# Kernel tuning notes

Hardware: AMD Instinct MI355X
Metric: run time of the kernel (lower is better)

The kernel has to match this reference:

```python
import jax, jax.numpy as jnp
import numpy as np

B, N, D = 16, 1024, 768
H = 12
HD = D // H           # 64
NUM_BUCKETS = 49      # iRPE 'product' buckets, shared across heads
SCALE = HD ** -0.5


def setup_inputs() -> dict:
    key = jax.random.key(0)
    k1, k2, k3, k4, k5, k6 = jax.random.split(key, 6)
    x = jax.random.normal(k1, (B, N, D), dtype=jnp.float32)
    qkv_w = jax.random.normal(k2, (3 * D, D), dtype=jnp.float32) * 0.02
    rpe_table = jax.random.normal(k3, (NUM_BUCKETS, HD), dtype=jnp.float32) * 0.02
    rp_bucket = jax.random.randint(k4, (N, N), 0, NUM_BUCKETS, dtype=jnp.int32)
    proj_w = jax.random.normal(k5, (D, D), dtype=jnp.float32) * 0.02
    proj_b = jax.random.normal(k6, (D,), dtype=jnp.float32) * 0.02
    return {"x": x, "qkv_w": qkv_w, "rpe_table": rpe_table,
            "rp_bucket": rp_bucket, "proj_w": proj_w, "proj_b": proj_b}


def reference(x, qkv_w, rpe_table, rp_bucket, proj_w, proj_b):
    b, n, d = x.shape
    # qkv projection (no bias), split into q,k,v of shape [B,H,N,HD]
    qkv = (x @ qkv_w.T).reshape(b, n, 3, H, HD)
    qkv = jnp.transpose(qkv, (2, 0, 3, 1, 4))
    q, k, v = qkv[0], qkv[1], qkv[2]
    q = q * SCALE
    # full attention scores [B,H,N,N]
    attn = jnp.einsum('bhid,bhjd->bhij', q, k)
    # iRPE contextual bias on keys: project q onto the bucket table, then
    # gather per relative-position bucket: bias[b,h,i,j] = (q @ W^T)[b,h,i,rp_bucket[i,j]]
    bias_all = jnp.einsum('bhid,cd->bhic', q, rpe_table)   # [B,H,N,num_buckets]
    bias = bias_all[:, :, jnp.arange(n)[:, None], rp_bucket]  # [B,H,N,N]
    attn = jax.nn.softmax(attn + bias, axis=-1)
    out = jnp.einsum('bhij,bhjd->bhid', attn, v)            # [B,H,N,HD]
    out = jnp.transpose(out, (0, 2, 1, 3)).reshape(b, n, d)
    return out @ proj_w.T + proj_b
```

## Files before the change

kernel.cpp:

```cpp
#include <hip/hip_runtime.h>

typedef short bf16x8 __attribute__((ext_vector_type(8)));
typedef float f32x4 __attribute__((ext_vector_type(4)));

#define QSCALE 0.1803368801111204f

__device__ __forceinline__ unsigned short f2bf(float f){
  unsigned u = __float_as_uint(f);
  u = (u + 0x7fffu + ((u >> 16) & 1u)) >> 16;
  return (unsigned short)u;
}
__device__ __forceinline__ f32x4 mfma16(bf16x8 a, bf16x8 b, f32x4 c){
  return __builtin_amdgcn_mfma_f32_16x16x32_bf16(a, b, c, 0, 0, 0);
}
__device__ __forceinline__ void gload_lds16(const void* g, void* l){
  __builtin_amdgcn_global_load_lds((__attribute__((address_space(1))) void*)(g),
                                   (__attribute__((address_space(3))) void*)(l), 16, 0, 0);
}
__device__ __forceinline__ unsigned cvt_pk_bf16(float lo, float hi){
  unsigned r;
  asm("v_cvt_pk_bf16_f32 %0, %1, %2" : "=v"(r) : "v"(lo), "v"(hi));
  return r;
}
__device__ __forceinline__ float exp2_fast(float x){
  float r;
  asm("v_exp_f32 %0, %1" : "=v"(r) : "v"(x));
  return r;
}

__global__ __launch_bounds__(256) void prep_kernel(
    const float* __restrict__ x, const float* __restrict__ qw,
    const float* __restrict__ pw, const int* __restrict__ rp,
    unsigned short* __restrict__ xb, unsigned short* __restrict__ wb,
    unsigned short* __restrict__ pwb, unsigned char* __restrict__ rp8){
  const int T1 = 3145728;
  const int T2 = T1 + 442368;
  const int T3 = T2 + 147456;
  const int T4 = T3 + 262144;
  for (int t = blockIdx.x * 256 + threadIdx.x; t < T4; t += gridDim.x * 256){
    if (t < T3){
      const float4* src; ushort4* dst; int off;
      if (t < T1){ src = (const float4*)x;  dst = (ushort4*)xb;  off = t; }
      else if (t < T2){ src = (const float4*)qw; dst = (ushort4*)wb;  off = t - T1; }
      else { src = (const float4*)pw; dst = (ushort4*)pwb; off = t - T2; }
      float4 v = src[off];
      ushort4 u;
      u.x = f2bf(v.x); u.y = f2bf(v.y); u.z = f2bf(v.z); u.w = f2bf(v.w);
      dst[off] = u;
    } else {
      int off = t - T3;
      int4 v = ((const int4*)rp)[off];
      int row = (off * 4) >> 10;
      int sw = (row & 7) << 4;
      uchar4 u;
      u.x = (unsigned char)((v.x << 2) ^ sw);
      u.y = (unsigned char)((v.y << 2) ^ sw);
      u.z = (unsigned char)((v.z << 2) ^ sw);
      u.w = (unsigned char)((v.w << 2) ^ sw);
      ((uchar4*)rp8)[off] = u;
    }
  }
}

__device__ __forceinline__ void gemm_core(
    const unsigned short* __restrict__ A, const unsigned short* __restrict__ Bm,
    int m0, int n0, int K, unsigned short* As, unsigned short* Bs,
    f32x4 (&acc)[4][4]){
  const int tid = threadIdx.x, lane = tid & 63, wave = tid >> 6;
  const int g = lane >> 4, r16 = lane & 15;
  const int wr = wave >> 1, wc = wave & 1;
  for (int k0 = 0; k0 < K; k0 += 32){
    __syncthreads();
    #pragma unroll
    for (int j = 0; j < 2; j++){
      int ci = j * 256 + tid;
      int row = ci >> 2, c = ci & 3;
      gload_lds16(A  + (size_t)(m0 + row) * K + k0 + c * 8,
                  (char*)As + (j * 256 + wave * 64) * 16);
      gload_lds16(Bm + (size_t)(n0 + row) * K + k0 + c * 8,
                  (char*)Bs + (j * 256 + wave * 64) * 16);
    }
    __syncthreads();
    bf16x8 a[4], b[4];
    #pragma unroll
    for (int mi = 0; mi < 4; mi++)
      a[mi] = *(const bf16x8*)((const char*)As + (wr * 64 + mi * 16 + r16) * 64 + g * 16);
    #pragma unroll
    for (int ni = 0; ni < 4; ni++)
      b[ni] = *(const bf16x8*)((const char*)Bs + (wc * 64 + ni * 16 + r16) * 64 + g * 16);
    #pragma unroll
    for (int mi = 0; mi < 4; mi++)
      #pragma unroll
      for (int ni = 0; ni < 4; ni++)
        acc[mi][ni] = mfma16(a[mi], b[ni], acc[mi][ni]);
  }
}

__global__ __launch_bounds__(256) void qkv_gemm(
    const unsigned short* __restrict__ xb, const unsigned short* __restrict__ wb,
    unsigned short* __restrict__ q_s, unsigned short* __restrict__ k_s,
    unsigned short* __restrict__ v_t){
  __shared__ __align__(16) unsigned short As[128 * 32];
  __shared__ __align__(16) unsigned short Bs[128 * 32];
  f32x4 acc[4][4];
  #pragma unroll
  for (int i = 0; i < 4; i++)
    #pragma unroll
    for (int j = 0; j < 4; j++){
      acc[i][j][0] = 0.f; acc[i][j][1] = 0.f; acc[i][j][2] = 0.f; acc[i][j][3] = 0.f;
    }
  const int m0 = blockIdx.y * 128, n0 = blockIdx.x * 128;
  gemm_core(xb, wb, m0, n0, 768, As, Bs, acc);

  const int lane = threadIdx.x & 63, wave = threadIdx.x >> 6;
  const int g = lane >> 4, r16 = lane & 15;
  const int wr = wave >> 1, wc = wave & 1;
  #pragma unroll
  for (int mi = 0; mi < 4; mi++){
    #pragma unroll
    for (int ni = 0; ni < 4; ni++){
      int gcol = n0 + wc * 64 + ni * 16 + r16;
      int sel = gcol / 768;
      int rem = gcol - sel * 768;
      int h = rem >> 6, hd = rem & 63;
      #pragma unroll
      for (int r = 0; r < 4; r++){
        int grow = m0 + wr * 64 + mi * 16 + 4 * g + r;
        int bb = grow >> 10, ii = grow & 1023;
        size_t base = ((size_t)(bb * 12 + h)) << 16;
        float v = acc[mi][ni][r];
        if (sel == 0)      q_s[base + ((size_t)ii << 6) + hd] = f2bf(v * QSCALE);
        else if (sel == 1) k_s[base + ((size_t)ii << 6) + hd] = f2bf(v);
        else               v_t[base + ((size_t)hd << 10) + ii] = f2bf(v);
      }
    }
  }
}

__global__ __launch_bounds__(256) void attn_kernel(
    const unsigned short* __restrict__ q_s, const unsigned short* __restrict__ k_s,
    const unsigned short* __restrict__ v_t, const unsigned char* __restrict__ rp8,
    const float* __restrict__ rpe, unsigned short* __restrict__ ao){
  __shared__ __align__(16) char smem[40960];
  const int tid = threadIdx.x, lane = tid & 63, w = tid >> 6;
  const int g = lane >> 4, r16 = lane & 15;
  const int qb = blockIdx.x, bh = blockIdx.y;
  const size_t bh_base = (size_t)bh << 16;

  const int i_loc = w * 16 + r16;
  const size_t qoff = bh_base + ((size_t)(qb * 64 + i_loc) << 6);
  bf16x8 qf0 = *(const bf16x8*)(q_s + qoff + g * 8);
  bf16x8 qf1 = *(const bf16x8*)(q_s + qoff + 32 + g * 8);

  float* bias_lds = (float*)(smem + 24576);
  const int s4 = (i_loc & 7) << 2;
  #pragma unroll
  for (int jt = 0; jt < 4; jt++){
    int row = jt * 16 + r16;
    bf16x8 a0, a1;
    #pragma unroll
    for (int e = 0; e < 8; e++){ a0[e] = 0; a1[e] = 0; }
    if (row < 49){
      const float* rr = rpe + row * 64 + g * 8;
      float4 x0 = *(const float4*)(rr);
      float4 x1 = *(const float4*)(rr + 4);
      float4 y0 = *(const float4*)(rr + 32);
      float4 y1 = *(const float4*)(rr + 36);
      a0[0]=f2bf(x0.x); a0[1]=f2bf(x0.y); a0[2]=f2bf(x0.z); a0[3]=f2bf(x0.w);
      a0[4]=f2bf(x1.x); a0[5]=f2bf(x1.y); a0[6]=f2bf(x1.z); a0[7]=f2bf(x1.w);
      a1[0]=f2bf(y0.x); a1[1]=f2bf(y0.y); a1[2]=f2bf(y0.z); a1[3]=f2bf(y0.w);
      a1[4]=f2bf(y1.x); a1[5]=f2bf(y1.y); a1[6]=f2bf(y1.z); a1[7]=f2bf(y1.w);
    }
    f32x4 z = {0.f, 0.f, 0.f, 0.f};
    z = mfma16(a0, qf0, z);
    z = mfma16(a1, qf1, z);
    *(f32x4*)(bias_lds + i_loc * 64 + ((jt * 16 + 4 * g) ^ s4)) = z;
  }

  unsigned short* ks = (unsigned short*)smem;
  unsigned short* vs = (unsigned short*)(smem + 8192);
  char* pbuf = smem + 16384 + w * 2048;
  const char* browb = (const char*)bias_lds + i_loc * 256;

  const int ci0 = tid, ci1 = 256 + tid;
  const int row0 = ci0 >> 3, sc0 = (ci0 & 7) ^ (row0 & 7);
  const int row1 = ci1 >> 3, sc1 = (ci1 & 7) ^ (row1 & 7);
  const char* kp0 = (const char*)(k_s + bh_base) + row0 * 128 + sc0 * 16;
  const char* kp1 = (const char*)(k_s + bh_base) + row1 * 128 + sc1 * 16;
  const char* vp0 = (const char*)(v_t + bh_base) + row0 * 2048 + sc0 * 16;
  const char* vp1 = (const char*)(v_t + bh_base) + row1 * 2048 + sc1 * 16;
  char* kl0 = (char*)smem + w * 1024;
  char* kl1 = (char*)smem + 4096 + w * 1024;
  char* vl0 = (char*)smem + 8192 + w * 1024;
  char* vl1 = (char*)smem + 12288 + w * 1024;
  const unsigned char* rprow = rp8 + ((size_t)(qb * 64 + i_loc) << 10);

  f32x4 o[4];
  #pragma unroll
  for (int dt = 0; dt < 4; dt++){ o[dt][0]=0.f; o[dt][1]=0.f; o[dt][2]=0.f; o[dt][3]=0.f; }
  float m_i = -INFINITY, l_i = 0.f;

  for (int kb = 0; kb < 16; kb++){
    __syncthreads();
    gload_lds16(kp0, kl0);
    gload_lds16(kp1, kl1);
    gload_lds16(vp0, vl0);
    gload_lds16(vp1, vl1);
    kp0 += 8192; kp1 += 8192; vp0 += 128; vp1 += 128;
    __syncthreads();

    f32x4 st[4];
    #pragma unroll
    for (int jt = 0; jt < 4; jt++){
      int krow = jt * 16 + r16;
      int sw = (krow & 7) << 4;
      bf16x8 ka0 = *(const bf16x8*)((char*)ks + krow * 128 + ((g * 16) ^ sw));
      bf16x8 ka1 = *(const bf16x8*)((char*)ks + krow * 128 + ((64 + g * 16) ^ sw));
      f32x4 z = {0.f, 0.f, 0.f, 0.f};
      z = mfma16(ka0, qf0, z);
      z = mfma16(ka1, qf1, z);
      st[jt] = z;
    }
    #pragma unroll
    for (int jt = 0; jt < 4; jt++){
      unsigned bu = *(const unsigned*)(rprow + kb * 64 + jt * 16 + g * 4);
      st[jt][0] += *(const float*)(browb + (bu & 0xff));
      st[jt][1] += *(const float*)(browb + ((bu >> 8) & 0xff));
      st[jt][2] += *(const float*)(browb + ((bu >> 16) & 0xff));
      st[jt][3] += *(const float*)(browb + (bu >> 24));
    }
    float tmax = -INFINITY;
    #pragma unroll
    for (int jt = 0; jt < 4; jt++)
      tmax = fmaxf(tmax, fmaxf(fmaxf(st[jt][0], st[jt][1]), fmaxf(st[jt][2], st[jt][3])));
    tmax = fmaxf(tmax, __shfl_xor(tmax, 16));
    tmax = fmaxf(tmax, __shfl_xor(tmax, 32));
    const bool skip = __all(tmax <= m_i + 8.f);
    float mnew = m_i, alpha;
    if (!skip){
      mnew = fmaxf(m_i, tmax);
      alpha = exp2_fast(m_i - mnew);
    }
    float psum = 0.f;
    #pragma unroll
    for (int jt = 0; jt < 4; jt++){
      float p0 = exp2_fast(st[jt][0] - mnew);
      float p1 = exp2_fast(st[jt][1] - mnew);
      float p2 = exp2_fast(st[jt][2] - mnew);
      float p3 = exp2_fast(st[jt][3] - mnew);
      psum += (p0 + p1) + (p2 + p3);
      uint2 u; u.x = cvt_pk_bf16(p0, p1); u.y = cvt_pk_bf16(p2, p3);
      *(uint2*)(pbuf + r16 * 128 + ((jt * 32 + g * 8) ^ ((r16 & 7) << 4))) = u;
    }
    psum += __shfl_xor(psum, 16);
    psum += __shfl_xor(psum, 32);
    if (!skip){
      l_i = l_i * alpha + psum;
      float af[4];
      #pragma unroll
      for (int r = 0; r < 4; r++) af[r] = __shfl(alpha, 4 * g + r);
      #pragma unroll
      for (int dt = 0; dt < 4; dt++){
        o[dt][0] *= af[0]; o[dt][1] *= af[1]; o[dt][2] *= af[2]; o[dt][3] *= af[3];
      }
    } else {
      l_i += psum;
    }
    m_i = mnew;
    #pragma unroll
    for (int kt = 0; kt < 2; kt++){
      bf16x8 pa = *(const bf16x8*)(pbuf + r16 * 128 + ((kt * 64 + g * 16) ^ ((r16 & 7) << 4)));
      #pragma unroll
      for (int dt = 0; dt < 4; dt++){
        int vrow = dt * 16 + r16;
        bf16x8 vb = *(const bf16x8*)((char*)vs + vrow * 128 + ((kt * 64 + g * 16) ^ ((vrow & 7) << 4)));
        o[dt] = mfma16(pa, vb, o[dt]);
      }
    }
  }

  float lf[4];
  #pragma unroll
  for (int r = 0; r < 4; r++) lf[r] = 1.f / __shfl(l_i, 4 * g + r);
  const int bidx = bh / 12, h = bh - bidx * 12;
  #pragma unroll
  for (int dt = 0; dt < 4; dt++){
    int d = dt * 16 + r16;
    #pragma unroll
    for (int r = 0; r < 4; r++){
      int i = qb * 64 + w * 16 + 4 * g + r;
      ao[(size_t)(bidx * 1024 + i) * 768 + h * 64 + d] = f2bf(o[dt][r] * lf[r]);
    }
  }
}

__global__ __launch_bounds__(256) void proj_gemm(
    const unsigned short* __restrict__ aob, const unsigned short* __restrict__ pwb,
    const float* __restrict__ pb, float* __restrict__ out){
  __shared__ __align__(16) unsigned short As[128 * 32];
  __shared__ __align__(16) unsigned short Bs[128 * 32];
  f32x4 acc[4][4];
  #pragma unroll
  for (int i = 0; i < 4; i++)
    #pragma unroll
    for (int j = 0; j < 4; j++){
      acc[i][j][0] = 0.f; acc[i][j][1] = 0.f; acc[i][j][2] = 0.f; acc[i][j][3] = 0.f;
    }
  const int m0 = blockIdx.y * 128, n0 = blockIdx.x * 128;
  gemm_core(aob, pwb, m0, n0, 768, As, Bs, acc);

  const int lane = threadIdx.x & 63, wave = threadIdx.x >> 6;
  const int g = lane >> 4, r16 = lane & 15;
  const int wr = wave >> 1, wc = wave & 1;
  #pragma unroll
  for (int mi = 0; mi < 4; mi++){
    #pragma unroll
    for (int ni = 0; ni < 4; ni++){
      int gcol = n0 + wc * 64 + ni * 16 + r16;
      float bias = pb[gcol];
      #pragma unroll
      for (int r = 0; r < 4; r++){
        int grow = m0 + wr * 64 + mi * 16 + 4 * g + r;
        out[(size_t)grow * 768 + gcol] = acc[mi][ni][r] + bias;
      }
    }
  }
}

extern "C" void kernel_launch(void* const* d_in, const int* in_sizes, int n_in,
                              void* d_out, int out_size, void* d_ws, size_t ws_size,
                              hipStream_t stream){
  const float* x      = (const float*)d_in[0];
  const float* qkv_w  = (const float*)d_in[1];
  const float* rpe    = (const float*)d_in[2];
  const int*   rp     = (const int*)d_in[3];
  const float* proj_w = (const float*)d_in[4];
  const float* proj_b = (const float*)d_in[5];
  float* out = (float*)d_out;
  char* ws = (char*)d_ws;

  unsigned short* xb  = (unsigned short*)(ws);
  unsigned short* wb  = (unsigned short*)(ws + 25165824);
  unsigned short* pwb = (unsigned short*)(ws + 28704768);
  unsigned char*  rp8 = (unsigned char*) (ws + 29884416);
  unsigned short* q_s = (unsigned short*)(ws + 30932992);
  unsigned short* k_s = (unsigned short*)(ws + 56098816);
  unsigned short* v_t = (unsigned short*)(ws + 81264640);
  unsigned short* aob = (unsigned short*)(ws + 106430464);

  prep_kernel<<<2048, 256, 0, stream>>>(x, qkv_w, proj_w, rp, xb, wb, pwb, rp8);
  qkv_gemm<<<dim3(18, 128), 256, 0, stream>>>(xb, wb, q_s, k_s, v_t);
  attn_kernel<<<dim3(16, 192), 256, 0, stream>>>(q_s, k_s, v_t, rp8, rpe, aob);
  proj_gemm<<<dim3(6, 128), 256, 0, stream>>>(aob, pwb, proj_b, out);
}
```

Baseline: 309.3 us.

## Process 32 query rows per wave in attention and store bias table as bf16

Each attention wave now handles two 16-row query tiles (128 queries per block, half as many blocks), so every K/V tile loaded into LDS is reused across twice as many queries, halving K/V global traffic and sync overhead per query. The per-row bucket bias table is stored in LDS as bf16 instead of fp32 (bucket indices pre-shifted by 1 instead of 2) so the larger query tile fits in LDS. The row-sum reduction is deferred to the end of the loop. Costs are more registers (8 accumulators, 4 Q fragments), larger LDS per block, fewer blocks for occupancy, and slightly lower bias precision.

New measurement: 307.1 us. About the same (-0.7%).

```diff
diff --git a/kernel.cpp b/kernel.cpp
--- a/kernel.cpp
+++ b/kernel.cpp
@@ -53,10 +53,10 @@
       int row = (off * 4) >> 10;
       int sw = (row & 7) << 4;
       uchar4 u;
-      u.x = (unsigned char)((v.x << 2) ^ sw);
-      u.y = (unsigned char)((v.y << 2) ^ sw);
-      u.z = (unsigned char)((v.z << 2) ^ sw);
-      u.w = (unsigned char)((v.w << 2) ^ sw);
+      u.x = (unsigned char)((v.x << 1) ^ sw);
+      u.y = (unsigned char)((v.y << 1) ^ sw);
+      u.z = (unsigned char)((v.z << 1) ^ sw);
+      u.w = (unsigned char)((v.w << 1) ^ sw);
       ((uchar4*)rp8)[off] = u;
     }
   }
@@ -141,27 +141,29 @@
     const unsigned short* __restrict__ q_s, const unsigned short* __restrict__ k_s,
     const unsigned short* __restrict__ v_t, const unsigned char* __restrict__ rp8,
     const float* __restrict__ rpe, unsigned short* __restrict__ ao){
-  __shared__ __align__(16) char smem[40960];
+  __shared__ __align__(16) char smem[49152];
   const int tid = threadIdx.x, lane = tid & 63, w = tid >> 6;
   const int g = lane >> 4, r16 = lane & 15;
   const int qb = blockIdx.x, bh = blockIdx.y;
   const size_t bh_base = (size_t)bh << 16;
-
-  const int i_loc = w * 16 + r16;
-  const size_t qoff = bh_base + ((size_t)(qb * 64 + i_loc) << 6);
-  bf16x8 qf0 = *(const bf16x8*)(q_s + qoff + g * 8);
-  bf16x8 qf1 = *(const bf16x8*)(q_s + qoff + 32 + g * 8);
-
-  float* bias_lds = (float*)(smem + 24576);
-  const int s4 = (i_loc & 7) << 2;
+  const int iw = w * 32;
+
+  const size_t q0 = bh_base + ((size_t)(qb * 128 + iw + r16) << 6);
+  bf16x8 qf[4];
+  qf[0] = *(const bf16x8*)(q_s + q0 + g * 8);
+  qf[1] = *(const bf16x8*)(q_s + q0 + 32 + g * 8);
+  qf[2] = *(const bf16x8*)(q_s + q0 + 1024 + g * 8);
+  qf[3] = *(const bf16x8*)(q_s + q0 + 1024 + 32 + g * 8);
+
+  char* bias_lds = smem + 32768;
   #pragma unroll
   for (int jt = 0; jt < 4; jt++){
-    int row = jt * 16 + r16;
+    int crow = jt * 16 + r16;
     bf16x8 a0, a1;
     #pragma unroll
     for (int e = 0; e < 8; e++){ a0[e] = 0; a1[e] = 0; }
-    if (row < 49){
-      const float* rr = rpe + row * 64 + g * 8;
+    if (crow < 49){
+      const float* rr = rpe + crow * 64 + g * 8;
       float4 x0 = *(const float4*)(rr);
       float4 x1 = *(const float4*)(rr + 4);
       float4 y0 = *(const float4*)(rr + 32);
@@ -171,16 +173,22 @@
       a1[0]=f2bf(y0.x); a1[1]=f2bf(y0.y); a1[2]=f2bf(y0.z); a1[3]=f2bf(y0.w);
       a1[4]=f2bf(y1.x); a1[5]=f2bf(y1.y); a1[6]=f2bf(y1.z); a1[7]=f2bf(y1.w);
     }
-    f32x4 z = {0.f, 0.f, 0.f, 0.f};
-    z = mfma16(a0, qf0, z);
-    z = mfma16(a1, qf1, z);
-    *(f32x4*)(bias_lds + i_loc * 64 + ((jt * 16 + 4 * g) ^ s4)) = z;
-  }
+    #pragma unroll
+    for (int h = 0; h < 2; h++){
+      f32x4 z = {0.f, 0.f, 0.f, 0.f};
+      z = mfma16(a0, qf[2 * h], z);
+      z = mfma16(a1, qf[2 * h + 1], z);
+      int irow = iw + h * 16 + r16;
+      uint2 u; u.x = cvt_pk_bf16(z[0], z[1]); u.y = cvt_pk_bf16(z[2], z[3]);
+      *(uint2*)(bias_lds + irow * 128 + ((jt * 32 + 8 * g) ^ ((r16 & 7) << 4))) = u;
+    }
+  }
+  const char* brow0 = bias_lds + (iw + r16) * 128;
+  const char* brow1 = brow0 + 16 * 128;
 
   unsigned short* ks = (unsigned short*)smem;
   unsigned short* vs = (unsigned short*)(smem + 8192);
-  char* pbuf = smem + 16384 + w * 2048;
-  const char* browb = (const char*)bias_lds + i_loc * 256;
+  char* pbuf = smem + 16384 + w * 4096;
 
   const int ci0 = tid, ci1 = 256 + tid;
   const int row0 = ci0 >> 3, sc0 = (ci0 & 7) ^ (row0 & 7);
@@ -193,12 +201,13 @@
   char* kl1 = (char*)smem + 4096 + w * 1024;
   char* vl0 = (char*)smem + 8192 + w * 1024;
   char* vl1 = (char*)smem + 12288 + w * 1024;
-  const unsigned char* rprow = rp8 + ((size_t)(qb * 64 + i_loc) << 10);
-
-  f32x4 o[4];
-  #pragma unroll
-  for (int dt = 0; dt < 4; dt++){ o[dt][0]=0.f; o[dt][1]=0.f; o[dt][2]=0.f; o[dt][3]=0.f; }
-  float m_i = -INFINITY, l_i = 0.f;
+  const unsigned char* rprow0 = rp8 + ((size_t)(qb * 128 + iw + r16) << 10);
+  const unsigned char* rprow1 = rprow0 + (16 << 10);
+
+  f32x4 o[8];
+  #pragma unroll
+  for (int t = 0; t < 8; t++){ o[t][0]=0.f; o[t][1]=0.f; o[t][2]=0.f; o[t][3]=0.f; }
+  float m0 = -INFINITY, m1 = -INFINITY, l0 = 0.f, l1 = 0.f;
 
   for (int kb = 0; kb < 16; kb++){
     __syncthreads();
@@ -209,87 +218,109 @@
     kp0 += 8192; kp1 += 8192; vp0 += 128; vp1 += 128;
     __syncthreads();
 
-    f32x4 st[4];
+    f32x4 st0[4], st1[4];
     #pragma unroll
     for (int jt = 0; jt < 4; jt++){
       int krow = jt * 16 + r16;
       int sw = (krow & 7) << 4;
       bf16x8 ka0 = *(const bf16x8*)((char*)ks + krow * 128 + ((g * 16) ^ sw));
       bf16x8 ka1 = *(const bf16x8*)((char*)ks + krow * 128 + ((64 + g * 16) ^ sw));
-      f32x4 z = {0.f, 0.f, 0.f, 0.f};
-      z = mfma16(ka0, qf0, z);
-      z = mfma16(ka1, qf1, z);
-      st[jt] = z;
+      f32x4 z0 = {0.f, 0.f, 0.f, 0.f};
+      z0 = mfma16(ka0, qf[0], z0);
+      z0 = mfma16(ka1, qf[1], z0);
+      st0[jt] = z0;
+      f32x4 z1 = {0.f, 0.f, 0.f, 0.f};
+      z1 = mfma16(ka0, qf[2], z1);
+      z1 = mfma16(ka1, qf[3], z1);
+      st1[jt] = z1;
     }
     #pragma unroll
     for (int jt = 0; jt < 4; jt++){
-      unsigned bu = *(const unsigned*)(rprow + kb * 64 + jt * 16 + g * 4);
-      st[jt][0] += *(const float*)(browb + (bu & 0xff));
-      st[jt][1] += *(const float*)(browb + ((bu >> 8) & 0xff));
-      st[jt][2] += *(const float*)(browb + ((bu >> 16) & 0xff));
-      st[jt][3] += *(const float*)(browb + (bu >> 24));
-    }
-    float tmax = -INFINITY;
-    #pragma unroll
-    for (int jt = 0; jt < 4; jt++)
-      tmax = fmaxf(tmax, fmaxf(fmaxf(st[jt][0], st[jt][1]), fmaxf(st[jt][2], st[jt][3])));
-    tmax = fmaxf(tmax, __shfl_xor(tmax, 16));
-    tmax = fmaxf(tmax, __shfl_xor(tmax, 32));
-    const bool skip = __all(tmax <= m_i + 8.f);
-    float mnew = m_i, alpha;
+      unsigned bu0 = *(const unsigned*)(rprow0 + kb * 64 + jt * 16 + g * 4);
+      unsigned bu1 = *(const unsigned*)(rprow1 + kb * 64 + jt * 16 + g * 4);
+      st0[jt][0] += __uint_as_float((unsigned)*(const unsigned short*)(brow0 + (bu0 & 0xff)) << 16);
+      st0[jt][1] += __uint_as_float((unsigned)*(const unsigned short*)(brow0 + ((bu0 >> 8) & 0xff)) << 16);
+      st0[jt][2] += __uint_as_float((unsigned)*(const unsigned short*)(brow0 + ((bu0 >> 16) & 0xff)) << 16);
+      st0[jt][3] += __uint_as_float((unsigned)*(const unsigned short*)(brow0 + (bu0 >> 24)) << 16);
+      st1[jt][0] += __uint_as_float((unsigned)*(const unsigned short*)(brow1 + (bu1 & 0xff)) << 16);
+      st1[jt][1] += __uint_as_float((unsigned)*(const unsigned short*)(brow1 + ((bu1 >> 8) & 0xff)) << 16);
+      st1[jt][2] += __uint_as_float((unsigned)*(const unsigned short*)(brow1 + ((bu1 >> 16) & 0xff)) << 16);
+      st1[jt][3] += __uint_as_float((unsigned)*(const unsigned short*)(brow1 + (bu1 >> 24)) << 16);
+    }
+    float t0 = -INFINITY, t1 = -INFINITY;
+    #pragma unroll
+    for (int jt = 0; jt < 4; jt++){
+      t0 = fmaxf(t0, fmaxf(fmaxf(st0[jt][0], st0[jt][1]), fmaxf(st0[jt][2], st0[jt][3])));
+      t1 = fmaxf(t1, fmaxf(fmaxf(st1[jt][0], st1[jt][1]), fmaxf(st1[jt][2], st1[jt][3])));
+    }
+    t0 = fmaxf(t0, __shfl_xor(t0, 16)); t0 = fmaxf(t0, __shfl_xor(t0, 32));
+    t1 = fmaxf(t1, __shfl_xor(t1, 16)); t1 = fmaxf(t1, __shfl_xor(t1, 32));
+    const bool skip = __all(t0 <= m0 + 8.f && t1 <= m1 + 8.f);
     if (!skip){
-      mnew = fmaxf(m_i, tmax);
-      alpha = exp2_fast(m_i - mnew);
-    }
-    float psum = 0.f;
+      float m0n = fmaxf(m0, t0), m1n = fmaxf(m1, t1);
+      float a0 = exp2_fast(m0 - m0n), a1 = exp2_fast(m1 - m1n);
+      m0 = m0n; m1 = m1n;
+      l0 *= a0; l1 *= a1;
+      float af0[4], af1[4];
+      #pragma unroll
+      for (int r = 0; r < 4; r++){ af0[r] = __shfl(a0, 4 * g + r); af1[r] = __shfl(a1, 4 * g + r); }
+      #pragma unroll
+      for (int dt = 0; dt < 4; dt++){
+        o[dt][0] *= af0[0]; o[dt][1] *= af0[1]; o[dt][2] *= af0[2]; o[dt][3] *= af0[3];
+        o[4+dt][0] *= af1[0]; o[4+dt][1] *= af1[1]; o[4+dt][2] *= af1[2]; o[4+dt][3] *= af1[3];
+      }
+    }
     #pragma unroll
     for (int jt = 0; jt < 4; jt++){
-      float p0 = exp2_fast(st[jt][0] - mnew);
-      float p1 = exp2_fast(st[jt][1] - mnew);
-      float p2 = exp2_fast(st[jt][2] - mnew);
-      float p3 = exp2_fast(st[jt][3] - mnew);
-      psum += (p0 + p1) + (p2 + p3);
+      float p0 = exp2_fast(st0[jt][0] - m0);
+      float p1 = exp2_fast(st0[jt][1] - m0);
+      float p2 = exp2_fast(st0[jt][2] - m0);
+      float p3 = exp2_fast(st0[jt][3] - m0);
+      l0 += (p0 + p1) + (p2 + p3);
       uint2 u; u.x = cvt_pk_bf16(p0, p1); u.y = cvt_pk_bf16(p2, p3);
       *(uint2*)(pbuf + r16 * 128 + ((jt * 32 + g * 8) ^ ((r16 & 7) << 4))) = u;
-    }
-    psum += __shfl_xor(psum, 16);
-    psum += __shfl_xor(psum, 32);
-    if (!skip){
-      l_i = l_i * alpha + psum;
-      float af[4];
-      #pragma unroll
-      for (int r = 0; r < 4; r++) af[r] = __shfl(alpha, 4 * g + r);
-      #pragma unroll
-      for (int dt = 0; dt < 4; dt++){
-        o[dt][0] *= af[0]; o[dt][1] *= af[1]; o[dt][2] *= af[2]; o[dt][3] *= af[3];
-      }
-    } else {
-      l_i += psum;
-    }
-    m_i = mnew;
+      float q0_ = exp2_fast(st1[jt][0] - m1);
+      float q1_ = exp2_fast(st1[jt][1] - m1);
+      float q2_ = exp2_fast(st1[jt][2] - m1);
+      float q3_ = exp2_fast(st1[jt][3] - m1);
+      l1 += (q0_ + q1_) + (q2_ + q3_);
+      uint2 v; v.x = cvt_pk_bf16(q0_, q1_); v.y = cvt_pk_bf16(q2_, q3_);
+      *(uint2*)(pbuf + (16 + r16) * 128 + ((jt * 32 + g * 8) ^ ((r16 & 7) << 4))) = v;
+    }
     #pragma unroll
     for (int kt = 0; kt < 2; kt++){
-      bf16x8 pa = *(const bf16x8*)(pbuf + r16 * 128 + ((kt * 64 + g * 16) ^ ((r16 & 7) << 4)));
+      bf16x8 pa0 = *(const bf16x8*)(pbuf + r16 * 128 + ((kt * 64 + g * 16) ^ ((r16 & 7) << 4)));
+      bf16x8 pa1 = *(const bf16x8*)(pbuf + (16 + r16) * 128 + ((kt * 64 + g * 16) ^ ((r16 & 7) << 4)));
       #pragma unroll
       for (int dt = 0; dt < 4; dt++){
         int vrow = dt * 16 + r16;
         bf16x8 vb = *(const bf16x8*)((char*)vs + vrow * 128 + ((kt * 64 + g * 16) ^ ((vrow & 7) << 4)));
-        o[dt] = mfma16(pa, vb, o[dt]);
-      }
-    }
-  }
-
-  float lf[4];
-  #pragma unroll
-  for (int r = 0; r < 4; r++) lf[r] = 1.f / __shfl(l_i, 4 * g + r);
-  const int bidx = bh / 12, h = bh - bidx * 12;
-  #pragma unroll
-  for (int dt = 0; dt < 4; dt++){
-    int d = dt * 16 + r16;
-    #pragma unroll
-    for (int r = 0; r < 4; r++){
-      int i = qb * 64 + w * 16 + 4 * g + r;
-      ao[(size_t)(bidx * 1024 + i) * 768 + h * 64 + d] = f2bf(o[dt][r] * lf[r]);
+        o[dt] = mfma16(pa0, vb, o[dt]);
+        o[4+dt] = mfma16(pa1, vb, o[4+dt]);
+      }
+    }
+  }
+
+  l0 += __shfl_xor(l0, 16); l0 += __shfl_xor(l0, 32);
+  l1 += __shfl_xor(l1, 16); l1 += __shfl_xor(l1, 32);
+  float lf0[4], lf1[4];
+  #pragma unroll
+  for (int r = 0; r < 4; r++){
+    lf0[r] = 1.f / __shfl(l0, 4 * g + r);
+    lf1[r] = 1.f / __shfl(l1, 4 * g + r);
+  }
+  const int bidx = bh / 12, hh = bh - bidx * 12;
+  #pragma unroll
+  for (int h = 0; h < 2; h++){
+    #pragma unroll
+    for (int dt = 0; dt < 4; dt++){
+      int d = dt * 16 + r16;
+      #pragma unroll
+      for (int r = 0; r < 4; r++){
+        int i = qb * 128 + iw + h * 16 + 4 * g + r;
+        float val = o[h * 4 + dt][r] * (h ? lf1[r] : lf0[r]);
+        ao[(size_t)(bidx * 1024 + i) * 768 + hh * 64 + d] = f2bf(val);
+      }
     }
   }
 }
@@ -350,6 +381,6 @@
 
   prep_kernel<<<2048, 256, 0, stream>>>(x, qkv_w, proj_w, rp, xb, wb, pwb, rp8);
   qkv_gemm<<<dim3(18, 128), 256, 0, stream>>>(xb, wb, q_s, k_s, v_t);
-  attn_kernel<<<dim3(16, 192), 256, 0, stream>>>(q_s, k_s, v_t, rp8, rpe, aob);
+  attn_kernel<<<dim3(8, 192), 256, 0, stream>>>(q_s, k_s, v_t, rp8, rpe, aob);
   proj_gemm<<<dim3(6, 128), 256, 0, stream>>>(aob, pwb, proj_b, out);
 }
```
